# Kernel optimization log

Hardware: AMD Instinct MI355X
Metric: run time of the kernel (lower is better)

The kernel has to match this reference:

```python
import jax, jax.numpy as jnp
import numpy as np

B, NQ, C = 4, 3136, 512
H_IMG, W_IMG = 56, 56
HEADS, D_MODEL, D_K, D_V = 8, 512, 512, 512
RATIO = 2
LN_EPS = 1e-3   # keras LayerNormalization default
BN_EPS = 1e-3   # keras BatchNormalization default


def setup_inputs() -> dict:
    key = jax.random.key(0)
    ks = jax.random.split(key, 16)
    s = 0.02
    inp = {
        'queries': jax.random.normal(ks[0], (B, NQ, C), jnp.float32),
        'keys': jax.random.normal(ks[1], (B, NQ, C), jnp.float32),
        'values': jax.random.normal(ks[2], (B, NQ, C), jnp.float32),
        'Wq': jax.random.normal(ks[3], (C, HEADS * D_K), jnp.float32) * s,
        'bq': jnp.zeros((HEADS * D_K,), jnp.float32),
        'Wk': jax.random.normal(ks[4], (C, HEADS * D_K), jnp.float32) * s,
        'bk': jnp.zeros((HEADS * D_K,), jnp.float32),
        'Wv': jax.random.normal(ks[5], (C, HEADS * D_V), jnp.float32) * s,
        'bv': jnp.zeros((HEADS * D_V,), jnp.float32),
        'Wo': jax.random.normal(ks[6], (HEADS * D_V, D_MODEL), jnp.float32) * s,
        'bo': jnp.zeros((D_MODEL,), jnp.float32),
        # depthwise conv: kernel (kh, kw, in_per_group=1, out=C)
        'sr_kernel': jax.random.normal(ks[7], (RATIO + 1, RATIO + 1, 1, C), jnp.float32) * s,
        'sr_bias': jnp.zeros((C,), jnp.float32),
        'ln_gamma': jnp.ones((C,), jnp.float32),
        'ln_beta': jnp.zeros((C,), jnp.float32),
        # 1x1 channels_first conv over the head axis of the score tensor
        'tw': jax.random.normal(ks[8], (HEADS, HEADS), jnp.float32) * s,
        'tb': jnp.zeros((HEADS,), jnp.float32),
        # BatchNormalization(axis=[0,1]) -> params per (batch, head)
        'bn_gamma': jnp.ones((B, HEADS), jnp.float32),
        'bn_beta': jnp.zeros((B, HEADS), jnp.float32),
    }
    return inp


def _forward(queries, keys, values, Wq, bq, Wk, bk, Wv, bv, Wo, bo,
             sr_kernel, sr_bias, ln_gamma, ln_beta, tw, tb, bn_gamma, bn_beta):
    b, nq, c = queries.shape
    # Q projection -> (b, h, nq, d_model)  (d_k == d_model)
    q = (queries @ Wq + bq).reshape(b, nq, HEADS, D_MODEL).transpose(0, 2, 1, 3)
    # spatial reduction of K/V source (ratio > 1 path; keys/values args unused)
    x = queries.reshape(b, H_IMG, W_IMG, c)
    x = jax.lax.conv_general_dilated(
        x, sr_kernel, window_strides=(RATIO, RATIO), padding='SAME',
        dimension_numbers=('NHWC', 'HWIO', 'NHWC'), feature_group_count=c) + sr_bias
    x = x.reshape(b, -1, c)  # (b, nk, c), nk = (H/ratio)*(W/ratio)
    mu = jnp.mean(x, axis=-1, keepdims=True)
    var = jnp.mean(jnp.square(x - mu), axis=-1, keepdims=True)
    x = (x - mu) * jax.lax.rsqrt(var + LN_EPS) * ln_gamma + ln_beta
    k = (x @ Wk + bk).reshape(b, -1, HEADS, D_MODEL).transpose(0, 2, 1, 3)
    v = (x @ Wv + bv).reshape(b, -1, HEADS, D_MODEL).transpose(0, 2, 1, 3)
    # scores (b, h, nq, nk)
    att = jnp.einsum('bhqd,bhkd->bhqk', q, k) / np.sqrt(D_K).astype(np.float32)
    # transform: 1x1 conv over head channel, softmax over k, BN over (q, k)
    att = jnp.einsum('bhqk,hg->bgqk', att, tw) + tb[:, None, None]
    att = jax.nn.softmax(att, axis=-1)
    m = jnp.mean(att, axis=(2, 3), keepdims=True)
    s2 = jnp.mean(jnp.square(att - m), axis=(2, 3), keepdims=True)
    att = bn_gamma[:, :, None, None] * (att - m) * jax.lax.rsqrt(s2 + BN_EPS) \
          + bn_beta[:, :, None, None]
    # attend and project out
    out = jnp.einsum('bhqk,bhkd->bhqd', att, v)
    out = out.transpose(0, 2, 1, 3).reshape(b, nq, HEADS * D_V)
    return out @ Wo + bo


def reference(queries, keys, values, Wq, bq, Wk, bk, Wv, bv, Wo, bo,
              sr_kernel, sr_bias, ln_gamma, ln_beta, tw, tb, bn_gamma, bn_beta):
    return _forward(queries, keys, values, Wq, bq, Wk, bk, Wv, bv, Wo, bo,
                    sr_kernel, sr_bias, ln_gamma, ln_beta, tw, tb, bn_gamma, bn_beta)
```

## Files before the change

kernel.cpp:

```cpp
#include <hip/hip_runtime.h>
#include <hip/hip_bf16.h>
#include <math.h>

typedef unsigned short u16;
typedef __attribute__((ext_vector_type(4))) float f32x4;
typedef __attribute__((ext_vector_type(8))) __bf16 bf16x8;

#define B_    4
#define NQ_   3136
#define C_    512
#define HIMG  56
#define WIMG  56
#define HD_   4096
#define NK_   784
#define NKP_  832

static __device__ __forceinline__ float b2f(u16 u){
  union { unsigned int i; float f; } v; v.i = ((unsigned int)u)<<16; return v.f;
}
static __device__ __forceinline__ u16 f2b(float f){
  union { float f; unsigned int i; } v; v.f = f;
  unsigned int r = v.i + 0x7fffu + ((v.i>>16)&1u);
  return (u16)(r>>16);
}

#define GLD16(gsrc, ldst) __builtin_amdgcn_global_load_lds( \
    (const __attribute__((address_space(1))) void*)(gsrc), \
    (__attribute__((address_space(3))) void*)(ldst), 16, 0, 0)

static __device__ __forceinline__ long xcd_rank(long n){
  const long l = blockIdx.x + (long)gridDim.x*(blockIdx.y + (long)gridDim.y*blockIdx.z);
  const long q8 = n>>3, r8 = n&7;
  const long xcd = l&7, idx = l>>3;
  return (xcd<r8 ? xcd*(q8+1) : r8*(q8+1) + (xcd-r8)*q8) + idx;
}
static __device__ __forceinline__ void order_byinner(int &bx, int &by, int &bz){
  const int nx = gridDim.x, ny = gridDim.y, nz = gridDim.z;
  long g = xcd_rank((long)nx*ny*nz);
  by = (int)(g % ny); g /= ny;
  bx = (int)(g % nx);
  bz = (int)(g / nx);
}
static __device__ __forceinline__ void order_panel(int mp, int np, int &bx, int &by){
  const int nx = gridDim.x, ny = gridDim.y;
  int rem = (int)xcd_rank((long)nx*ny);
  int mi = 0, ni = 0;
  for(int p = 0; p < mp*np; p++){
    mi = p/np; ni = p%np;
    const int sx = nx/mp + (mi < nx%mp ? 1 : 0);
    const int sy = ny/np + (ni < ny%np ? 1 : 0);
    const int cnt = sx*sy;
    if(rem < cnt) break;
    rem -= cnt;
  }
  const int sy = ny/np + (ni < ny%np ? 1 : 0);
  const int basex = mi*(nx/mp) + (mi < nx%mp ? mi : nx%mp);
  const int basey = ni*(ny/np) + (ni < ny%np ? ni : ny%np);
  bx = basex + rem / sy;
  by = basey + rem % sy;
}

template<int OUT_F32>
__global__ __launch_bounds__(256, 2)
void gemm128(const u16* __restrict__ A, const u16* __restrict__ Bm, void* __restrict__ Cm,
             int M, int Ncols, int K, int sA, int sB, int sC, int zdiv,
             long long zA1, long long zA2, long long zB1, long long zB2,
             long long zC1, long long zC2,
             const float* __restrict__ bias1, float hscale,
             const float* __restrict__ scalePtr,
             const float* __restrict__ bias2, int rowsPerB, int b2s,
             int mp, int np)
{
  __shared__ u16 lds[36864];
  int bx, by, z;
  if(mp > 0){ order_panel(mp, np, bx, by); z = 0; }
  else      { order_byinner(bx, by, z); }
  const int zq = z / zdiv, zr = z % zdiv;
  const u16* Ab = A  + (long long)zq*zA1 + (long long)zr*zA2;
  const u16* Bb = Bm + (long long)zq*zB1 + (long long)zr*zB2;
  const int m0 = bx*256, n0 = by*128;
  const int t = threadIdx.x, w = t>>6, lane = t&63;
  const int wm = w>>1, wn = w&1;
  const int l15 = lane & 15;

  const int srow = t>>2;
  const int scol = (((t&3) ^ ((srow>>1)&3)) << 3);
  const u16* aS = Ab + (long long)(m0 + srow)*sA + scol;
  const u16* bS = Bb + (long long)(n0 + srow)*sB + scol;
  const long long sA64 = (long long)64*sA, sB64 = (long long)64*sB;
  const int w512 = w*512;

#define STAGE(jt, buf) do{                                        \
    const u16* a0_ = aS + (long long)(jt)*32;                     \
    const u16* b0_ = bS + (long long)(jt)*32;                     \
    u16* la_ = lds + (buf)*8192 + w512;                           \
    u16* lb_ = lds + 24576 + (buf)*4096 + w512;                   \
    GLD16(a0_,          la_);                                     \
    GLD16(a0_ +   sA64, la_ + 2048);                              \
    GLD16(a0_ + 2*sA64, la_ + 4096);                              \
    GLD16(a0_ + 3*sA64, la_ + 6144);                              \
    GLD16(b0_,          lb_);                                     \
    GLD16(b0_ +   sB64, lb_ + 2048);                              \
  }while(0)

  f32x4 acc[8][4];
#pragma unroll
  for(int i=0;i<8;i++)
#pragma unroll
    for(int j=0;j<4;j++) acc[i][j] = (f32x4)(0.0f);

  const char* ldsc = (const char*)lds;
  const int ck = (((lane>>4) ^ ((lane>>1)&3)) << 4);
  const int aRowB = (wm*128 + l15) * 64;
  const int bRowB = (wn*64  + l15) * 64;

  const int T = K >> 5;
  STAGE(0, 0);
  STAGE(1, 1);

  int buf = 0;
  for(int j=0; j<T; j++){
    if(j == T-1) asm volatile("s_waitcnt vmcnt(0)" ::: "memory");
    else         asm volatile("s_waitcnt vmcnt(6)" ::: "memory");
    asm volatile("s_barrier" ::: "memory");

    const int aBuf = buf*16384 + aRowB;
    const int bBuf = 49152 + buf*8192 + bRowB;
    bf16x8 af[8], bfv[4];
#pragma unroll
    for(int fr=0; fr<8; fr++) af[fr]  = *(const bf16x8*)(ldsc + aBuf + fr*1024 + ck);
#pragma unroll
    for(int fn=0; fn<4; fn++) bfv[fn] = *(const bf16x8*)(ldsc + bBuf + fn*1024 + ck);
    {
      const int nbuf = (buf+2 >= 3) ? buf-1 : buf+2;
      if(j+2 < T) STAGE(j+2, nbuf);
    }
    __builtin_amdgcn_s_setprio(1);
#pragma unroll
    for(int fr=0; fr<8; fr++)
#pragma unroll
      for(int fn=0; fn<4; fn++)
        acc[fr][fn] = __builtin_amdgcn_mfma_f32_16x16x32_bf16(af[fr], bfv[fn], acc[fr][fn], 0,0,0);
    __builtin_amdgcn_s_setprio(0);
    buf = (buf+1 >= 3) ? 0 : buf+1;
  }
#undef STAGE

  const float dsc = scalePtr ? scalePtr[z] : 1.0f;
  const long long cBase = (long long)zq*zC1 + (long long)zr*zC2;
  const int r4 = (lane>>4)*4;
#pragma unroll
  for(int mf=0; mf<8; mf++){
    const int row0 = m0 + wm*128 + mf*16 + r4;
#pragma unroll
    for(int nf=0; nf<4; nf++){
      const int col = n0 + wn*64 + nf*16 + l15;
      if(col < Ncols){
#pragma unroll
        for(int r=0;r<4;r++){
          const int row = row0 + r;
          if(row < M){
            float v = acc[mf][nf][r];
            if(bias1) v += bias1[col];
            v *= hscale * dsc;
            if(bias2) v += bias2[(row/rowsPerB)*b2s + col];
            if(OUT_F32) ((float*)Cm)[cBase + (long long)row*sC + col] = v;
            else        ((u16*) Cm)[cBase + (long long)row*sC + col] = f2b(v);
          }
        }
      }
    }
  }
}

__global__ __launch_bounds__(256)
void wt_kernel(const float* __restrict__ W, u16* __restrict__ Wt, int K, int N){
  __shared__ float tile[32][33];
  const int n0 = blockIdx.x*32, k0 = blockIdx.y*32;
  const int t = threadIdx.x, tr = t>>5, tc = t&31;
#pragma unroll
  for(int i=0;i<4;i++)
    tile[tr+i*8][tc] = W[(long long)(k0+tr+i*8)*N + n0+tc];
  __syncthreads();
#pragma unroll
  for(int i=0;i<4;i++)
    Wt[(long long)(n0+tr+i*8)*K + k0+tc] = f2b(tile[tc][tr+i*8]);
}

__global__ __launch_bounds__(256)
void cvt_bf16(const float* __restrict__ in, u16* __restrict__ outp, long long n){
  long long i = ((long long)blockIdx.x*256 + threadIdx.x)*4;
  if(i+3 < n){
    float4 v = *(const float4*)(in+i);
    ushort4 o; o.x=f2b(v.x); o.y=f2b(v.y); o.z=f2b(v.z); o.w=f2b(v.w);
    *(ushort4*)(outp+i) = o;
  }
}

__global__ __launch_bounds__(256)
void conv_ln(const float* __restrict__ q, const float* __restrict__ ker,
             const float* __restrict__ cbias, const float* __restrict__ gamma,
             const float* __restrict__ beta, u16* __restrict__ xo)
{
  const int p = blockIdx.x;
  const int b = p / 784, pix = p % 784;
  const int oy = pix / 28, ox = pix % 28;
  const int t = threadIdx.x;
  __shared__ float red[256];
  float v[2];
#pragma unroll
  for(int e=0;e<2;e++){
    const int c = t + e*256;
    float acc = cbias[c];
    for(int ky=0;ky<3;ky++){
      const int y = oy*2 + ky;
      if(y >= HIMG) continue;
      for(int kx=0;kx<3;kx++){
        const int x = ox*2 + kx;
        if(x >= WIMG) continue;
        acc += q[(((long long)b*HIMG + y)*WIMG + x)*C_ + c] * ker[(ky*3+kx)*C_ + c];
      }
    }
    v[e] = acc;
  }
  red[t]=v[0]+v[1]; __syncthreads();
  for(int st=128; st>0; st>>=1){ if(t<st) red[t]+=red[t+st]; __syncthreads(); }
  const float mu = red[0] * (1.0f/C_);
  __syncthreads();
  const float d0=v[0]-mu, d1=v[1]-mu;
  red[t]=d0*d0+d1*d1; __syncthreads();
  for(int st=128; st>0; st>>=1){ if(t<st) red[t]+=red[t+st]; __syncthreads(); }
  const float rs = rsqrtf(red[0]*(1.0f/C_) + 1e-3f);
  const long long ob = (long long)p*C_;
#pragma unroll
  for(int e=0;e<2;e++){
    const int c = t+e*256;
    xo[ob+c] = f2b((v[e]-mu)*rs*gamma[c] + beta[c]);
  }
}

__global__ __launch_bounds__(256)
void vt_kernel(const u16* __restrict__ Vf_b, u16* __restrict__ Vt_b, int sV){
  __shared__ u16 tile[32][33];
  const int k0 = blockIdx.x*32, d0 = blockIdx.y*32;
  const int t = threadIdx.x, tr = t>>5, tc = t&31;
#pragma unroll
  for(int i=0;i<4;i++){
    const int k = k0+tr+i*8;
    tile[tr+i*8][tc] = (k < NK_) ? Vf_b[(long long)k*sV + d0+tc] : (u16)0;
  }
  __syncthreads();
#pragma unroll
  for(int i=0;i<4;i++)
    Vt_b[(long long)(d0+tr+i*8)*NKP_ + k0+tc] = tile[tc][tr+i*8];
}

__global__ __launch_bounds__(512)
void mix_softmax(u16* __restrict__ S_b, const float* __restrict__ tw,
                 float* __restrict__ partial_b)
{
  const int qi = blockIdx.x;
  const int t = threadIdx.x;
  const int wave = t >> 6, lane = t & 63;
  __shared__ float sv[8*NK_];
  const long long rowstr = (long long)NQ_*NKP_;
  const long long base = (long long)qi*NKP_;

  for(int idx = t; idx < 8*196; idx += 512){
    const int h = idx / 196, c4 = idx % 196;
    ushort4 u4 = *(const ushort4*)(S_b + base + h*rowstr + c4*4);
    float* d = sv + h*NK_ + c4*4;
    d[0]=b2f(u4.x); d[1]=b2f(u4.y); d[2]=b2f(u4.z); d[3]=b2f(u4.w);
  }
  __syncthreads();

  const int g = wave;
  float wgt[8];
#pragma unroll
  for(int h=0;h<8;h++) wgt[h] = tw[h*8+g];

  float xs[13];
  float lmax = -1e30f;
#pragma unroll
  for(int j=0;j<13;j++){
    const int k = j*64 + lane;
    if(k < NK_){
      float x = 0.f;
#pragma unroll
      for(int h=0;h<8;h++) x += wgt[h]*sv[h*NK_+k];
      xs[j] = x;
      lmax = fmaxf(lmax, x);
    } else xs[j] = -1e30f;
  }
#pragma unroll
  for(int off=32; off>=1; off>>=1) lmax = fmaxf(lmax, __shfl_xor(lmax, off));

  float lsum = 0.f;
#pragma unroll
  for(int j=0;j<13;j++){
    const int k = j*64 + lane;
    if(k < NK_){
      const float e = __expf(xs[j] - lmax);
      xs[j] = e; lsum += e;
    }
  }
#pragma unroll
  for(int off=32; off>=1; off>>=1) lsum += __shfl_xor(lsum, off);
  const float inv = 1.0f/lsum;

  u16* dst = S_b + base + g*rowstr;
  float lss = 0.f;
#pragma unroll
  for(int j=0;j<13;j++){
    const int k = j*64 + lane;
    if(k < NK_){
      const float dev = xs[j]*inv - (1.0f/NK_);
      dst[k] = f2b(dev);
      lss += dev*dev;
    }
  }
  for(int k = NK_ + lane; k < NKP_; k += 64) dst[k] = 0;
#pragma unroll
  for(int off=32; off>=1; off>>=1) lss += __shfl_xor(lss, off);
  if(lane==0) partial_b[g*NQ_ + qi] = lss;
}

__global__ __launch_bounds__(256)
void colsum_v(const u16* __restrict__ Vf_b, float* __restrict__ part, int sV){
  const int hd = blockIdx.x*256 + threadIdx.x;
  const int kc = blockIdx.y;
  const u16* p = Vf_b + (long long)kc*98*sV + hd;
  float s=0.f;
  for(int k=0;k<98;k++) s += b2f(p[(long long)k*sV]);
  part[(long long)kc*HD_ + hd] = s;
}

__global__ __launch_bounds__(256)
void finalize_stats(const float* __restrict__ partial_b, const float* __restrict__ bng_b,
                    const float* __restrict__ bnb_b, float* __restrict__ a_b,
                    float* __restrict__ c_b){
  const int g = blockIdx.x;
  const int t = threadIdx.x;
  __shared__ float red[4];
  float s = 0.f;
  for(int i=t; i<NQ_; i+=256) s += partial_b[g*NQ_ + i];
#pragma unroll
  for(int off=32; off>=1; off>>=1) s += __shfl_xor(s, off);
  if((t&63)==0) red[t>>6] = s;
  __syncthreads();
  if(t==0){
    const float tot = red[0]+red[1]+red[2]+red[3];
    const float s2 = tot * (1.0f/((float)NQ_*(float)NK_));
    a_b[g] = bng_b[g]*rsqrtf(s2 + 1e-3f);
    c_b[g] = bnb_b[g];
  }
}

__global__ __launch_bounds__(256)
void corr_kernel(const float* __restrict__ part, const u16* __restrict__ Wot,
                 const float* __restrict__ c_b, float* __restrict__ corr_b){
  const int n = blockIdx.x, t = threadIdx.x;
  __shared__ float red[256];
  float s = 0.f;
  for(int hd=t; hd<HD_; hd+=256){
    float cs = 0.f;
#pragma unroll
    for(int kc=0; kc<8; kc++) cs += part[(long long)kc*HD_ + hd];
    s += c_b[hd>>9] * cs * b2f(Wot[(long long)n*HD_+hd]);
  }
  red[t]=s; __syncthreads();
  for(int st=128; st>0; st>>=1){ if(t<st) red[t]+=red[t+st]; __syncthreads(); }
  if(t==0) corr_b[n]=red[0];
}

extern "C" void kernel_launch(void* const* d_in, const int* in_sizes, int n_in,
                              void* d_out, int out_size, void* d_ws, size_t ws_size,
                              hipStream_t stream)
{
  (void)in_sizes; (void)n_in; (void)out_size;
  const float* queries = (const float*)d_in[0];
  const float* Wq  = (const float*)d_in[3];
  const float* bq  = (const float*)d_in[4];
  const float* Wk  = (const float*)d_in[5];
  const float* bk  = (const float*)d_in[6];
  const float* Wv  = (const float*)d_in[7];
  const float* bv  = (const float*)d_in[8];
  const float* Wo  = (const float*)d_in[9];
  const float* bo  = (const float*)d_in[10];
  const float* srk = (const float*)d_in[11];
  const float* srb = (const float*)d_in[12];
  const float* lng = (const float*)d_in[13];
  const float* lnb = (const float*)d_in[14];
  const float* tw  = (const float*)d_in[15];
  const float* bng = (const float*)d_in[17];
  const float* bnb = (const float*)d_in[18];
  float* out = (float*)d_out;
  const float QSC = 0.04419417382415922f;

  char* w = (char*)d_ws;
  size_t off = 0;
  auto alloc = [&](size_t bytes)->char*{
    char* p = w + off; off += (bytes + 255) & ~(size_t)255; return p;
  };

  const bool tierA = (ws_size >= (size_t)210*1024*1024);

  u16* Wqt = (u16*)alloc((size_t)HD_*C_*2);
  u16* Wkt = (u16*)alloc((size_t)HD_*C_*2);
  u16* Wvt = (u16*)alloc((size_t)HD_*C_*2);
  u16* Wot = (u16*)alloc((size_t)C_*HD_*2);
  u16* x   = (u16*)alloc((size_t)B_*NK_*C_*2 + 262144);
  float* bkv = (float*)alloc((size_t)2*HD_*4);
  u16* Qin;
  u16* QfU;
  if(tierA){
    Qin = (u16*)alloc((size_t)B_*NQ_*C_*2);
    QfU = (u16*)alloc((size_t)B_*NQ_*HD_*2 + 2097152);
  } else {
    Qin = (u16*)alloc((size_t)NQ_*C_*2 + 262144);
    QfU = (u16*)alloc((size_t)NQ_*HD_*2 + 2097152);
  }
  u16* KV_b = (u16*)alloc((size_t)NK_*2*HD_*2 + 4194304);
  u16* Vt_b = (u16*)alloc((size_t)HD_*NKP_*2);
  u16* S_b  = (u16*)alloc((size_t)8*NQ_*NKP_*2 + 524288);
  float* colsum  = (float*)alloc((size_t)8*HD_*4);
  float* partial = (float*)alloc((size_t)8*NQ_*4);
  float* aArr    = (float*)alloc(256);
  float* cArr    = (float*)alloc(256);
  float* corrB   = (float*)alloc((size_t)B_*C_*4);

  wt_kernel<<<dim3(128,16), 256, 0, stream>>>(Wq, Wqt, 512, 4096);
  wt_kernel<<<dim3(128,16), 256, 0, stream>>>(Wk, Wkt, 512, 4096);
  wt_kernel<<<dim3(128,16), 256, 0, stream>>>(Wv, Wvt, 512, 4096);
  wt_kernel<<<dim3(16,128), 256, 0, stream>>>(Wo, Wot, 4096, 512);
  conv_ln<<<B_*NK_, 256, 0, stream>>>(queries, srk, srb, lng, lnb, x);
  hipMemcpyAsync(bkv,      bk, HD_*4, hipMemcpyDeviceToDevice, stream);
  hipMemcpyAsync(bkv+HD_,  bv, HD_*4, hipMemcpyDeviceToDevice, stream);

  if(tierA){
    cvt_bf16<<<6272, 256, 0, stream>>>(queries, Qin, (long long)B_*NQ_*C_);
    gemm128<0><<<dim3(49,32,1),256,0,stream>>>(Qin, Wqt, QfU, B_*NQ_, 4096, 512,
        512, 512, HD_, 1, 0,0,0,0,0,0, bq, QSC, nullptr, nullptr, 1, 0, 4, 2);
  }

  for(int b=0; b<B_; b++){
    u16* Qf_b = tierA ? (QfU + (size_t)b*NQ_*HD_) : QfU;
    if(!tierA){
      cvt_bf16<<<1568, 256, 0, stream>>>(queries + (size_t)b*NQ_*C_, Qin, (long long)NQ_*C_);
      gemm128<0><<<dim3(13,32,1),256,0,stream>>>(Qin, Wqt, Qf_b, NQ_, 4096, 512,
          512, 512, HD_, 1, 0,0,0,0,0,0, bq, QSC, nullptr, nullptr, 1, 0, 4, 2);
    }
    const u16* x_b = x + (size_t)b*NK_*C_;
    gemm128<0><<<dim3(4,64,1),256,0,stream>>>(x_b, Wkt, KV_b, NK_, 2*HD_, 512,
        512, 512, 2*HD_, 1, 0,0,0,0,0,0, bkv, 1.0f, nullptr, nullptr, 1, 0, 0, 0);
    vt_kernel<<<dim3(26,128),256,0,stream>>>(KV_b + HD_, Vt_b, 2*HD_);
    colsum_v<<<dim3(16,8),256,0,stream>>>(KV_b + HD_, colsum, 2*HD_);
    gemm128<0><<<dim3(13,7,8),256,0,stream>>>(Qf_b, KV_b, S_b, NQ_, NKP_, 512,
        HD_, 2*HD_, NKP_, 8, 0, 512, 0, 512, 0, (long long)NQ_*NKP_,
        nullptr, 1.0f, nullptr, nullptr, 1, 0, 0, 0);
    mix_softmax<<<NQ_, 512, 0, stream>>>(S_b, tw, partial);
    finalize_stats<<<8,256,0,stream>>>(partial, bng + b*8, bnb + b*8, aArr + b*8, cArr + b*8);
    corr_kernel<<<512,256,0,stream>>>(colsum, Wot, cArr + b*8, corrB + b*C_);
    gemm128<0><<<dim3(13,4,8),256,0,stream>>>(S_b, Vt_b, Qf_b, NQ_, 512, NKP_,
        NKP_, NKP_, HD_, 8, 0, (long long)NQ_*NKP_, 0, (long long)512*NKP_, 0, 512,
        nullptr, 1.0f, aArr + b*8, nullptr, 1, 0, 0, 0);
    if(!tierA){
      gemm128<1><<<dim3(13,4,1),256,0,stream>>>(Qf_b, Wot, out + (size_t)b*NQ_*C_,
          NQ_, 512, HD_, HD_, HD_, C_,
          1, 0,0,0,0,0,0, bo, 1.0f, nullptr, corrB + b*C_, NQ_, C_, 0, 0);
    }
  }

  if(tierA){
    gemm128<1><<<dim3(49,4,1),256,0,stream>>>(QfU, Wot, out, B_*NQ_, 512, HD_,
        HD_, HD_, C_, 1, 0,0,0,0,0,0, bo, 1.0f, nullptr, corrB, NQ_, C_, 0, 0);
  }
}
```

Before: 927.0 us.

## Add 256x256 eight-wave GEMM kernel with ping-pong staging for main GEMMs

Introduces a new GEMM kernel using 512-thread blocks computing 256x256 output tiles, with quarter-tile interleaved LDS staging, swizzled layout, barriers and s_setprio around MFMA bursts. It replaces the 128-tile kernel for the Q projection, score, attention-value and output GEMMs. The key padding grows from 832 to 896 so the score width fits whole 256 tiles. The larger tiles should raise data reuse per LDS load, at the cost of 128KB of LDS per block, one block per CU, more padded work and fewer blocks for the smaller grids.

```diff
diff --git a/kernel.cpp b/kernel.cpp
--- a/kernel.cpp
+++ b/kernel.cpp
@@ -13,7 +13,7 @@
 #define WIMG  56
 #define HD_   4096
 #define NK_   784
-#define NKP_  832
+#define NKP_  896
 
 static __device__ __forceinline__ float b2f(u16 u){
   union { unsigned int i; float f; } v; v.i = ((unsigned int)u)<<16; return v.f;
@@ -58,6 +58,163 @@
   const int basey = ni*(ny/np) + (ni < ny%np ? ni : ny%np);
   bx = basex + rem / sy;
   by = basey + rem % sy;
+}
+
+template<int OUT_F32>
+__global__ __launch_bounds__(512)
+void gemm8p(const u16* __restrict__ A, const u16* __restrict__ Bm, void* __restrict__ Cm,
+            int M, int Ncols, int K, int sA, int sB, int sC, int zdiv,
+            long long zA1, long long zA2, long long zB1, long long zB2,
+            long long zC1, long long zC2,
+            const float* __restrict__ bias1, float hscale,
+            const float* __restrict__ scalePtr,
+            const float* __restrict__ bias2, int rowsPerB, int b2s,
+            int mp, int np)
+{
+  __shared__ u16 lds[65536];
+  int bx, by, z;
+  if(mp > 0){ order_panel(mp, np, bx, by); z = 0; }
+  else      { order_byinner(bx, by, z); }
+  const int zq = z / zdiv, zr = z % zdiv;
+  const u16* Ab = A  + (long long)zq*zA1 + (long long)zr*zA2;
+  const u16* Bb = Bm + (long long)zq*zB1 + (long long)zr*zB2;
+  const int m0 = bx*256, n0 = by*256;
+  const int t = threadIdx.x, w = t>>6, lane = t&63;
+  const int wm = w>>2, wn = w&3;
+  const int l15 = lane & 15;
+
+  const int srow = t>>3;
+  const int scol = ((t&7)*8) ^ (((t>>5)&1)*16);
+  const u16* aS = Ab + (long long)(m0 + srow)*sA + scol;
+  const u16* bS = Bb + (long long)(n0 + srow)*sB + scol;
+  const long long sA64 = (long long)64*sA, sA128 = (long long)128*sA;
+  const long long sB64 = (long long)64*sB, sB128 = (long long)128*sB;
+  const int w512 = w*512;
+
+#define STAGE_A(tk, h) do{                                            \
+    const u16* s_ = aS + (long long)(h)*sA128 + (long long)(tk)*64;   \
+    u16* d_ = lds + ((((tk)&1)*2 + (h))*8192) + w512;                 \
+    GLD16(s_,        d_);                                             \
+    GLD16(s_ + sA64, d_ + 4096);                                      \
+  }while(0)
+#define STAGE_B(tk, h) do{                                            \
+    const u16* s_ = bS + (long long)(h)*sB128 + (long long)(tk)*64;   \
+    u16* d_ = lds + 32768 + ((((tk)&1)*2 + (h))*8192) + w512;         \
+    GLD16(s_,        d_);                                             \
+    GLD16(s_ + sB64, d_ + 4096);                                      \
+  }while(0)
+
+  f32x4 acc[8][4];
+#pragma unroll
+  for(int i=0;i<8;i++)
+#pragma unroll
+    for(int j=0;j<4;j++) acc[i][j] = (f32x4)(0.0f);
+
+  const char* ldsc = (const char*)lds;
+  const int swz5 = ((lane>>2)&1)<<5;
+  const int k0 = (0*64 + ((lane>>4)<<4)) ^ swz5;
+  const int k1 = (1*64 + ((lane>>4)<<4)) ^ swz5;
+  const int aHalfSel = wm;
+  const int bHalfSel = wn>>1;
+  const int bRow0 = (wn&1)*64;
+
+  bf16x8 af[4][2], bf[2][2][2];
+
+#define RD_A(qm) do{                                                        \
+    const int base_ = aSlot + ((qm)*64 + l15)*128;                          \
+    _Pragma("unroll")                                                       \
+    for(int fr=0; fr<4; fr++){                                              \
+      af[fr][0] = *(const bf16x8*)(ldsc + base_ + fr*16*128 + k0);          \
+      af[fr][1] = *(const bf16x8*)(ldsc + base_ + fr*16*128 + k1);          \
+    }                                                                       \
+  }while(0)
+#define RD_B(qn) do{                                                        \
+    const int base_ = bSlot + (bRow0 + (qn)*32 + l15)*128;                  \
+    _Pragma("unroll")                                                       \
+    for(int fn=0; fn<2; fn++){                                              \
+      bf[qn][fn][0] = *(const bf16x8*)(ldsc + base_ + fn*16*128 + k0);      \
+      bf[qn][fn][1] = *(const bf16x8*)(ldsc + base_ + fn*16*128 + k1);      \
+    }                                                                       \
+  }while(0)
+#define MM(qm,qn) do{                                                       \
+    _Pragma("unroll")                                                       \
+    for(int fr=0; fr<4; fr++)                                               \
+      _Pragma("unroll")                                                     \
+      for(int fn=0; fn<2; fn++){                                            \
+        f32x4 t_ = acc[(qm)*4+fr][(qn)*2+fn];                               \
+        t_ = __builtin_amdgcn_mfma_f32_16x16x32_bf16(af[fr][0], bf[qn][fn][0], t_, 0,0,0); \
+        t_ = __builtin_amdgcn_mfma_f32_16x16x32_bf16(af[fr][1], bf[qn][fn][1], t_, 0,0,0); \
+        acc[(qm)*4+fr][(qn)*2+fn] = t_;                                     \
+      }                                                                     \
+  }while(0)
+#define BAR()   asm volatile("s_barrier" ::: "memory")
+#define LGK0()  do{ asm volatile("s_waitcnt lgkmcnt(0)" ::: "memory"); \
+                    __builtin_amdgcn_sched_barrier(0); }while(0)
+
+  const int T = K >> 6;
+  STAGE_A(0,0); STAGE_A(0,1); STAGE_B(0,0); STAGE_B(0,1);
+  STAGE_B(1,0); STAGE_A(1,0);
+  asm volatile("s_waitcnt vmcnt(4)" ::: "memory");
+  BAR();
+
+  for(int tk=0; tk<T; tk++){
+    const int aSlot = ((tk&1)*2 + aHalfSel)*16384;
+    const int bSlot = 65536 + ((tk&1)*2 + bHalfSel)*16384;
+    RD_A(0); RD_B(0);
+    if(tk+1 < T) STAGE_B(tk+1, 1);
+    BAR(); LGK0();
+    __builtin_amdgcn_s_setprio(1); MM(0,0); __builtin_amdgcn_s_setprio(0);
+    BAR();
+    RD_B(1);
+    if(tk+1 < T) STAGE_A(tk+1, 1);
+    BAR(); LGK0();
+    __builtin_amdgcn_s_setprio(1); MM(0,1); __builtin_amdgcn_s_setprio(0);
+    BAR();
+    RD_A(1);
+    if(tk+2 < T) STAGE_B(tk+2, 0);
+    BAR(); LGK0();
+    __builtin_amdgcn_s_setprio(1); MM(1,0); __builtin_amdgcn_s_setprio(0);
+    BAR();
+    if(tk+2 < T) STAGE_A(tk+2, 0);
+    if(tk+1 < T){
+      if(tk+2 < T) asm volatile("s_waitcnt vmcnt(4)" ::: "memory");
+      else         asm volatile("s_waitcnt vmcnt(0)" ::: "memory");
+    }
+    BAR();
+    __builtin_amdgcn_s_setprio(1); MM(1,1); __builtin_amdgcn_s_setprio(0);
+    BAR();
+  }
+#undef RD_A
+#undef RD_B
+#undef MM
+#undef STAGE_A
+#undef STAGE_B
+
+  const float dsc = scalePtr ? scalePtr[z] : 1.0f;
+  const long long cBase = (long long)zq*zC1 + (long long)zr*zC2;
+  const int r4 = (lane>>4)*4;
+#pragma unroll
+  for(int mf=0; mf<8; mf++){
+    const int row0 = m0 + wm*128 + mf*16 + r4;
+#pragma unroll
+    for(int nf=0; nf<4; nf++){
+      const int col = n0 + wn*64 + nf*16 + l15;
+      if(col < Ncols){
+#pragma unroll
+        for(int r=0;r<4;r++){
+          const int row = row0 + r;
+          if(row < M){
+            float v = acc[mf][nf][r];
+            if(bias1) v += bias1[col];
+            v *= hscale * dsc;
+            if(bias2) v += bias2[(row/rowsPerB)*b2s + col];
+            if(OUT_F32) ((float*)Cm)[cBase + (long long)row*sC + col] = v;
+            else        ((u16*) Cm)[cBase + (long long)row*sC + col] = f2b(v);
+          }
+        }
+      }
+    }
+  }
 }
 
 template<int OUT_F32>
@@ -439,7 +596,7 @@
 
   if(tierA){
     cvt_bf16<<<6272, 256, 0, stream>>>(queries, Qin, (long long)B_*NQ_*C_);
-    gemm128<0><<<dim3(49,32,1),256,0,stream>>>(Qin, Wqt, QfU, B_*NQ_, 4096, 512,
+    gemm8p<0><<<dim3(49,16,1),512,0,stream>>>(Qin, Wqt, QfU, B_*NQ_, 4096, 512,
         512, 512, HD_, 1, 0,0,0,0,0,0, bq, QSC, nullptr, nullptr, 1, 0, 4, 2);
   }
 
@@ -447,32 +604,32 @@
     u16* Qf_b = tierA ? (QfU + (size_t)b*NQ_*HD_) : QfU;
     if(!tierA){
       cvt_bf16<<<1568, 256, 0, stream>>>(queries + (size_t)b*NQ_*C_, Qin, (long long)NQ_*C_);
-      gemm128<0><<<dim3(13,32,1),256,0,stream>>>(Qin, Wqt, Qf_b, NQ_, 4096, 512,
+      gemm8p<0><<<dim3(13,16,1),512,0,stream>>>(Qin, Wqt, Qf_b, NQ_, 4096, 512,
           512, 512, HD_, 1, 0,0,0,0,0,0, bq, QSC, nullptr, nullptr, 1, 0, 4, 2);
     }
     const u16* x_b = x + (size_t)b*NK_*C_;
     gemm128<0><<<dim3(4,64,1),256,0,stream>>>(x_b, Wkt, KV_b, NK_, 2*HD_, 512,
         512, 512, 2*HD_, 1, 0,0,0,0,0,0, bkv, 1.0f, nullptr, nullptr, 1, 0, 0, 0);
-    vt_kernel<<<dim3(26,128),256,0,stream>>>(KV_b + HD_, Vt_b, 2*HD_);
+    vt_kernel<<<dim3(28,128),256,0,stream>>>(KV_b + HD_, Vt_b, 2*HD_);
     colsum_v<<<dim3(16,8),256,0,stream>>>(KV_b + HD_, colsum, 2*HD_);
-    gemm128<0><<<dim3(13,7,8),256,0,stream>>>(Qf_b, KV_b, S_b, NQ_, NKP_, 512,
+    gemm8p<0><<<dim3(13,4,8),512,0,stream>>>(Qf_b, KV_b, S_b, NQ_, NKP_, 512,
         HD_, 2*HD_, NKP_, 8, 0, 512, 0, 512, 0, (long long)NQ_*NKP_,
         nullptr, 1.0f, nullptr, nullptr, 1, 0, 0, 0);
     mix_softmax<<<NQ_, 512, 0, stream>>>(S_b, tw, partial);
     finalize_stats<<<8,256,0,stream>>>(partial, bng + b*8, bnb + b*8, aArr + b*8, cArr + b*8);
     corr_kernel<<<512,256,0,stream>>>(colsum, Wot, cArr + b*8, corrB + b*C_);
-    gemm128<0><<<dim3(13,4,8),256,0,stream>>>(S_b, Vt_b, Qf_b, NQ_, 512, NKP_,
+    gemm8p<0><<<dim3(13,2,8),512,0,stream>>>(S_b, Vt_b, Qf_b, NQ_, 512, NKP_,
         NKP_, NKP_, HD_, 8, 0, (long long)NQ_*NKP_, 0, (long long)512*NKP_, 0, 512,
         nullptr, 1.0f, aArr + b*8, nullptr, 1, 0, 0, 0);
     if(!tierA){
-      gemm128<1><<<dim3(13,4,1),256,0,stream>>>(Qf_b, Wot, out + (size_t)b*NQ_*C_,
+      gemm8p<1><<<dim3(13,2,1),512,0,stream>>>(Qf_b, Wot, out + (size_t)b*NQ_*C_,
           NQ_, 512, HD_, HD_, HD_, C_,
           1, 0,0,0,0,0,0, bo, 1.0f, nullptr, corrB + b*C_, NQ_, C_, 0, 0);
     }
   }
 
   if(tierA){
-    gemm128<1><<<dim3(49,4,1),256,0,stream>>>(QfU, Wot, out, B_*NQ_, 512, HD_,
+    gemm8p<1><<<dim3(49,2,1),512,0,stream>>>(QfU, Wot, out, B_*NQ_, 512, HD_,
         HD_, HD_, C_, 1, 0,0,0,0,0,0, bo, 1.0f, nullptr, corrB, NQ_, C_, 0, 0);
   }
 }
```

Measured after the change: 1.084 ms. 16.9% more time.
